# Performance work log

Hardware: AMD Instinct MI355X
Metric: run time of the kernel (lower is better)

## Reference

```python
import jax, jax.numpy as jnp
import numpy as np

B, S, D, H = 2, 4096, 1024, 16
HD = D // H
KCONV = 4


def _rmsnorm(x, scale, eps=1e-6):
    return x * jax.lax.rsqrt(jnp.mean(x * x, axis=-1, keepdims=True) + eps) * scale


def _l2norm(x, eps=1e-6):
    return x * jax.lax.rsqrt(jnp.sum(x * x, axis=-1, keepdims=True) + eps)


def _causal_dwconv_silu(x, w):
    # x: [B,S,D], w: [D,K] depthwise taps (tap K-1 multiplies x[t])
    k = w.shape[1]
    s = x.shape[1]
    xp = jnp.pad(x, ((0, 0), (k - 1, 0), (0, 0)))
    out = sum(xp[:, i:i + s, :] * w[:, i] for i in range(k))
    return jax.nn.silu(out)


def _p20_scan(x, decay_log, theta):
    # BLOCK_DIAGONAL_2 rotary-state linear recurrence: channels paired into
    # complex state, s_t = a * s_{t-1} + u_t with a = exp(-exp(decay_log) + i*theta).
    b, s, d = x.shape
    xc = x.reshape(b, s, d // 2, 2)
    u = jax.lax.complex(xc[..., 0], xc[..., 1])  # [B,S,D/2]
    a = jnp.exp(-jnp.exp(decay_log)) * jnp.exp(1j * theta)  # [D/2] complex, |a|<1

    def step(carry, u_t):
        st = carry * a + u_t
        return st, st

    _, ys = jax.lax.scan(step, jnp.zeros((b, d // 2), u.dtype), jnp.swapaxes(u, 0, 1))
    ys = jnp.swapaxes(ys, 0, 1)  # [B,S,D/2]
    return jnp.stack([ys.real, ys.imag], axis=-1).reshape(b, s, d)


def _gated_delta_rule(q, k, v, g, beta):
    # q,k,v: [B,S,H,Dh]; g,beta: [B,S,H]. State S: [B,H,K,V].
    scale = q.shape[-1] ** -0.5
    q = _l2norm(q)
    k = _l2norm(k)
    qt, kt, vt = (jnp.moveaxis(t, 1, 0) for t in (q, k, v))
    gt, bt = (jnp.moveaxis(t, 1, 0) for t in (g, beta))
    s0 = jnp.zeros((q.shape[0], q.shape[2], q.shape[3], v.shape[3]), v.dtype)

    def step(state, inp):
        q_t, k_t, v_t, g_t, b_t = inp
        state = state * jnp.exp(g_t)[..., None, None]
        v_err = (v_t - jnp.einsum('bhkv,bhk->bhv', state, k_t)) * b_t[..., None]
        state = state + jnp.einsum('bhk,bhv->bhkv', k_t, v_err)
        o_t = jnp.einsum('bhkv,bhk->bhv', state, q_t) * scale
        return state, o_t

    _, o = jax.lax.scan(step, s0, (qt, kt, vt, gt, bt))
    return jnp.moveaxis(o, 0, 1)  # [B,S,H,V]


def setup_inputs() -> dict:
    key = jax.random.key(0)
    ks = jax.random.split(key, 16)
    w = lambda k, shp, s=0.02: (jax.random.normal(k, shp, jnp.float32) * s)
    ctrl_out = 3 * D + 2 * H + D  # q,k,v,decay,beta,output_gate
    ctrl_b = jnp.concatenate([
        jnp.zeros((3 * D,), jnp.float32),
        jnp.full((H,), 1.5, jnp.float32),       # decay bias
        jnp.full((H,), -2.0, jnp.float32),      # beta bias
        jnp.full((D,), -1.5, jnp.float32),      # output gate bias
    ])
    # depthwise conv init: delta at last tap + small noise
    def conv_w(k):
        base = jnp.zeros((D, KCONV), jnp.float32).at[:, -1].set(1.0)
        return base + w(k, (D, KCONV), 0.02)
    return {
        'hidden': jax.random.normal(ks[0], (B, S, D), jnp.float32),
        'p20_decay_log': w(ks[1], (D // 2,), 1.0),
        'p20_theta': jax.random.uniform(ks[2], (D // 2,), jnp.float32, 0.0, 2.0 * np.pi),
        'ctrl_W': w(ks[3], (D, ctrl_out)),
        'ctrl_b': ctrl_b,
        'p20c_W': w(ks[4], (D, 3 * D), 0.001),  # 0.05-scaled init
        'qconv_w': conv_w(ks[5]),
        'kconv_w': conv_w(ks[6]),
        'vconv_w': conv_w(ks[7]),
        'mnorm_scale': jnp.ones((HD,), jnp.float32),
        'vnorm_scale': jnp.ones((D,), jnp.float32),
        'ramp_logit': jnp.full((D,), -4.595, jnp.float32),  # logit(0.01)
        'out_W': w(ks[8], (2 * D, D), 0.02),
        'out_b': jnp.zeros((D,), jnp.float32),
    }


def reference(hidden, p20_decay_log, p20_theta, ctrl_W, ctrl_b, p20c_W,
              qconv_w, kconv_w, vconv_w, mnorm_scale, vnorm_scale,
              ramp_logit, out_W, out_b):
    b, s, d = hidden.shape
    # P20 vector-state side channel
    p20_read = _p20_scan(hidden, p20_decay_log, p20_theta)
    normed_p20 = _rmsnorm(p20_read, vnorm_scale)
    p20_q, p20_k, p20_v = jnp.split(normed_p20 @ p20c_W, 3, axis=-1)
    ramp = jax.nn.sigmoid(ramp_logit)  # [D]
    # packed control projection
    ctrl = hidden @ ctrl_W + ctrl_b
    q_in, k_in, v_in, dec_in, beta_in, gate_in = jnp.split(
        ctrl, np.cumsum([d, d, d, H, H]).tolist(), axis=-1)
    # causal depthwise conv + SiLU
    q_in = _causal_dwconv_silu(q_in, qconv_w)
    k_in = _causal_dwconv_silu(k_in, kconv_w)
    v_in = _causal_dwconv_silu(v_in, vconv_w)
    # P20-conditioned heads
    queries = (q_in + ramp * p20_q).reshape(b, s, H, HD)
    keys = (k_in + ramp * p20_k).reshape(b, s, H, HD)
    values = (v_in + ramp * p20_v).reshape(b, s, H, HD)
    g = jax.nn.log_sigmoid(dec_in.astype(jnp.float32)).astype(hidden.dtype)  # [B,S,H]
    beta = jax.nn.sigmoid(beta_in)
    reads = _gated_delta_rule(queries, keys, values, g, beta)
    normed_reads = _rmsnorm(reads, mnorm_scale).reshape(b, s, d)
    fused = jnp.concatenate([normed_reads, normed_p20], axis=-1)
    projected = fused @ out_W + out_b
    return jax.nn.sigmoid(gate_in) * projected
```

## Files before the change

kernel.cpp:

```cpp
#include <hip/hip_runtime.h>
#include <hip/hip_bf16.h>
#include <stdint.h>

#define SEQ  4096
#define NH   16
#define HD   64

typedef __attribute__((ext_vector_type(8))) short bf16x8;
typedef __attribute__((ext_vector_type(4))) float f32x4;

__device__ __forceinline__ float bf2f(unsigned short u){
  union{unsigned u;float f;} v; v.u = ((unsigned)u)<<16; return v.f;
}
__device__ __forceinline__ unsigned short f2bf(float f){
  union{float f;unsigned u;} v; v.f=f;
  return (unsigned short)((v.u + 0x7fffu + ((v.u>>16)&1u))>>16);
}
__device__ __forceinline__ float sigm(float x){ return 1.f/(1.f+__expf(-x)); }
__device__ __forceinline__ f32x4 mfma16(bf16x8 a, bf16x8 b, f32x4 c){
  return __builtin_amdgcn_mfma_f32_16x16x32_bf16(a,b,c,0,0,0);
}
__device__ __forceinline__ void gll16(const void* g, void* l){
  __builtin_amdgcn_global_load_lds((const __attribute__((address_space(1))) void*)g,
                                   (__attribute__((address_space(3))) void*)l, 16, 0, 0);
}

__global__ void k_fill(float* __restrict__ p, float v, long n){
  long i = (long)blockIdx.x*blockDim.x + threadIdx.x;
  long stride = (long)gridDim.x*blockDim.x;
  for (; i<n; i+=stride) p[i] = v;
}

__global__ void k_cvt_bf16(const float* __restrict__ in, unsigned short* __restrict__ out){
  long i = ((long)blockIdx.x*256 + threadIdx.x)*4;
  float4 v = *(const float4*)(in+i);
  ushort4 o; o.x=f2bf(v.x); o.y=f2bf(v.y); o.z=f2bf(v.z); o.w=f2bf(v.w);
  *(ushort4*)(out+i) = o;
}

__global__ void k_transpose(const float* __restrict__ in, unsigned short* __restrict__ out,
                            int R, int Cin, int Cpad){
  __shared__ float t[32][33];
  int cb = blockIdx.x*32, rb = blockIdx.y*32;
  int tx = threadIdx.x & 31, ty = threadIdx.x >> 5;
  for (int k=0;k<32;k+=8){
    int r = rb+ty+k, c = cb+tx;
    t[ty+k][tx] = (c<Cin) ? in[(long)r*Cin + c] : 0.f;
  }
  __syncthreads();
  for (int k=0;k<32;k+=8){
    int c = cb+ty+k, r = rb+tx;
    if (c<Cpad) out[(long)c*R + r] = f2bf(t[tx][ty+k]);
  }
}

#define FOR16(F) F(0,0) F(0,1) F(0,2) F(0,3) F(1,0) F(1,1) F(1,2) F(1,3) \
                 F(2,0) F(2,1) F(2,2) F(2,3) F(3,0) F(3,1) F(3,2) F(3,3)
#define FOR4(F) F(0) F(1) F(2) F(3)
#define ACC(i,j) Ac##i##j

#define GEMM_CORE(A_,lda_,Bt_,ldb_,K_)                                         \
  __shared__ unsigned short Ab[3][4096];                                       \
  __shared__ unsigned short Bb[3][4096];                                       \
  const int tid=threadIdx.x, wid=tid>>6, l=tid&63;                             \
  const long m0=(long)blockIdx.y*128, n0=(long)blockIdx.x*128;                 \
  const int nk=(K_)>>5;                                                        \
  const int wm=(wid>>1)*64, wn=(wid&1)*64;                                     \
  const int srow0 = tid>>2;                                                    \
  const int schunk = (((tid&3) ^ ((tid>>2)&3))<<3);              \
  const unsigned short* gA0 = (A_) + (m0+srow0)*(lda_) + schunk;               \
  const unsigned short* gA1 = (A_) + (m0+64+srow0)*(lda_) + schunk;            \
  const unsigned short* gB0 = (Bt_) + (n0+srow0)*(ldb_) + schunk;              \
  const unsigned short* gB1 = (Bt_) + (n0+64+srow0)*(ldb_) + schunk;           \
  const int ldst0 = tid*16, ldst1 = 4096 + tid*16;    \
  f32x4 Ac00={0.f,0.f,0.f,0.f};                                                \
  f32x4 Ac01=Ac00,Ac02=Ac00,Ac03=Ac00,Ac10=Ac00,Ac11=Ac00,Ac12=Ac00,           \
        Ac13=Ac00,Ac20=Ac00,Ac21=Ac00,Ac22=Ac00,Ac23=Ac00,Ac30=Ac00,           \
        Ac31=Ac00,Ac32=Ac00,Ac33=Ac00;                                         \
                                            \
  gll16(gA0, (char*)&Ab[0][0]+ldst0); gll16(gA1, (char*)&Ab[0][0]+ldst1);      \
  gll16(gB0, (char*)&Bb[0][0]+ldst0); gll16(gB1, (char*)&Bb[0][0]+ldst1);      \
  gA0+=32; gA1+=32; gB0+=32; gB1+=32;                                          \
  gll16(gA0, (char*)&Ab[1][0]+ldst0); gll16(gA1, (char*)&Ab[1][0]+ldst1);      \
  gll16(gB0, (char*)&Bb[1][0]+ldst0); gll16(gB1, (char*)&Bb[1][0]+ldst1);      \
  gA0+=32; gA1+=32; gB0+=32; gB1+=32;                                          \
  int rb=0, sb=2;                                                              \
  const int sxor = (l&3)<<4;                                                   \
  const int rao0 = (wm+(l&15))*64 + (((l>>4)<<4) ^ sxor);                      \
  const int rbo0 = (wn+(l&15))*64 + (((l>>4)<<4) ^ sxor);                      \
  for (int kt=0; kt<nk; ++kt){                                                 \
    if (kt+1<nk) { asm volatile("s_waitcnt vmcnt(4)" ::: "memory"); }          \
    else         { asm volatile("s_waitcnt vmcnt(0)" ::: "memory"); }          \
    __builtin_amdgcn_sched_barrier(0);                                         \
    __builtin_amdgcn_s_barrier();                                              \
    __builtin_amdgcn_sched_barrier(0);                                         \
    if (kt+2<nk){                                                              \
      gll16(gA0, (char*)&Ab[sb][0]+ldst0); gll16(gA1, (char*)&Ab[sb][0]+ldst1);\
      gll16(gB0, (char*)&Bb[sb][0]+ldst0); gll16(gB1, (char*)&Bb[sb][0]+ldst1);\
      gA0+=32; gA1+=32; gB0+=32; gB1+=32;                                      \
    }                                                                          \
    const char* Apt=(const char*)&Ab[rb][0];                                   \
    const char* Bpt=(const char*)&Bb[rb][0];                                   \
    bf16x8 af0=*(const bf16x8*)(Apt+rao0);      bf16x8 bf0=*(const bf16x8*)(Bpt+rbo0);      \
    bf16x8 af1=*(const bf16x8*)(Apt+rao0+1024); bf16x8 bf1=*(const bf16x8*)(Bpt+rbo0+1024); \
    bf16x8 af2=*(const bf16x8*)(Apt+rao0+2048); bf16x8 bf2=*(const bf16x8*)(Bpt+rbo0+2048); \
    bf16x8 af3=*(const bf16x8*)(Apt+rao0+3072); bf16x8 bf3=*(const bf16x8*)(Bpt+rbo0+3072); \
    __builtin_amdgcn_s_setprio(1);                                             \
    Ac00=mfma16(af0,bf0,Ac00); Ac01=mfma16(af0,bf1,Ac01);                      \
    Ac02=mfma16(af0,bf2,Ac02); Ac03=mfma16(af0,bf3,Ac03);                      \
    Ac10=mfma16(af1,bf0,Ac10); Ac11=mfma16(af1,bf1,Ac11);                      \
    Ac12=mfma16(af1,bf2,Ac12); Ac13=mfma16(af1,bf3,Ac13);                      \
    Ac20=mfma16(af2,bf0,Ac20); Ac21=mfma16(af2,bf1,Ac21);                      \
    Ac22=mfma16(af2,bf2,Ac22); Ac23=mfma16(af2,bf3,Ac23);                      \
    Ac30=mfma16(af3,bf0,Ac30); Ac31=mfma16(af3,bf1,Ac31);                      \
    Ac32=mfma16(af3,bf2,Ac32); Ac33=mfma16(af3,bf3,Ac33);                      \
    __builtin_amdgcn_s_setprio(0);                                             \
    rb = (rb==2)?0:rb+1; sb = (sb==2)?0:sb+1;                                  \
  }

__global__ __launch_bounds__(256,2) void k_gemm(
  const unsigned short* __restrict__ A, int lda,
  const unsigned short* __restrict__ Bt, int ldb,
  unsigned short* Cb, float* Cf, int ldc,
  int K, int Nvalid,
  const float* __restrict__ bias,
  const unsigned short* __restrict__ gate, int gld)
{
  GEMM_CORE(A, lda, Bt, ldb, K)
#define EPI_GEN(mi,ni) {                                                       \
  const int gn=(int)n0+wn+ni*16+(l&15);                                        \
  if (gn<Nvalid){                                                              \
    _Pragma("unroll") for(int r=0;r<4;r++){                                    \
      const long gm=m0+wm+mi*16+((l>>4)<<2)+r;                                 \
      float v=ACC(mi,ni)[r];                                                   \
      if(bias) v+=bias[gn];                                                    \
      if(gate) v*=bf2f(gate[gm*gld+gn]);                                       \
      if(Cb) Cb[gm*ldc+gn]=f2bf(v); else Cf[gm*ldc+gn]=v; } } }
  FOR16(EPI_GEN)
#undef EPI_GEN
}

__global__ __launch_bounds__(256,2) void k_gemm_ctrl(
  const unsigned short* __restrict__ A, int lda,
  const unsigned short* __restrict__ Bt, int ldb,
  unsigned short* __restrict__ ctrl,
  float* __restrict__ gbuf, float* __restrict__ bbuf,
  unsigned short* __restrict__ gateb,
  const float* __restrict__ bias)
{
  GEMM_CORE(A, lda, Bt, ldb, 1024)
#define EPI_CTRL(mi,ni) {                                                      \
  const int gn=(int)n0+wn+ni*16+(l&15);                                        \
  if (gn<4128){                                                                \
    const float bs=bias[gn];                                                   \
    _Pragma("unroll") for(int r=0;r<4;r++){                                    \
      const long gm=m0+wm+mi*16+((l>>4)<<2)+r;                                 \
      float v=ACC(mi,ni)[r]+bs;                                                \
      if (gn<3072)      ctrl[gm*3072+gn]=f2bf(v);                              \
      else if (gn<3088) gbuf[gm*16+(gn-3072)]=                                 \
                          (v>=0.f)?-log1pf(__expf(-v)):(v-log1pf(__expf(v)));  \
      else if (gn<3104) bbuf[gm*16+(gn-3088)]=sigm(v);                         \
      else              gateb[gm*1024+(gn-3104)]=f2bf(sigm(v)); } } }
  FOR16(EPI_CTRL)
#undef EPI_CTRL
}

__global__ __launch_bounds__(256,2) void k_gemm_qkv(
  const unsigned short* __restrict__ A, int lda,
  const unsigned short* __restrict__ Bt, int ldb,
  const float* __restrict__ ramp,
  unsigned short* __restrict__ Qb, unsigned short* __restrict__ Kb,
  unsigned short* __restrict__ Vb)
{
  GEMM_CORE(A, lda, Bt, ldb, 1024)
  const int seg = (int)((n0 + wn) >> 10);
  unsigned short* Ob = (seg==0)?Qb:((seg==1)?Kb:Vb);
  const int dc0=((int)n0+wn+0*16+(l&15))&1023; const float sr0=sigm(ramp[dc0]);
  const int dc1=((int)n0+wn+1*16+(l&15))&1023; const float sr1=sigm(ramp[dc1]);
  const int dc2=((int)n0+wn+2*16+(l&15))&1023; const float sr2=sigm(ramp[dc2]);
  const int dc3=((int)n0+wn+3*16+(l&15))&1023; const float sr3=sigm(ramp[dc3]);
#define EPI_QKV(mi) {                                                          \
  _Pragma("unroll") for(int r=0;r<4;r++){                                      \
    const long gm=m0+wm+mi*16+((l>>4)<<2)+r;                                   \
    float v0=bf2f(Ob[gm*1024+dc0])+sr0*ACC(mi,0)[r];                           \
    float v1=bf2f(Ob[gm*1024+dc1])+sr1*ACC(mi,1)[r];                           \
    float v2=bf2f(Ob[gm*1024+dc2])+sr2*ACC(mi,2)[r];                           \
    float v3=bf2f(Ob[gm*1024+dc3])+sr3*ACC(mi,3)[r];                           \
    if (seg<2){                                                                \
      float ss=v0*v0+v1*v1+v2*v2+v3*v3;                                        \
      ss+=__shfl_xor(ss,1); ss+=__shfl_xor(ss,2);                              \
      ss+=__shfl_xor(ss,4); ss+=__shfl_xor(ss,8);                              \
      float rs=rsqrtf(ss+1e-6f); v0*=rs; v1*=rs; v2*=rs; v3*=rs; }             \
    Ob[gm*1024+dc0]=f2bf(v0); Ob[gm*1024+dc1]=f2bf(v1);                        \
    Ob[gm*1024+dc2]=f2bf(v2); Ob[gm*1024+dc3]=f2bf(v3); } }
  FOR4(EPI_QKV)
#undef EPI_QKV
}

__global__ void k_scan1(const float* __restrict__ hidden, const float* __restrict__ dlog,
                        const float* __restrict__ theta, float2* __restrict__ finals){
  int idx = blockIdx.x*256 + threadIdx.x;
  int ch = idx & 511; int chunk = (idx>>9) & 63; int b = idx>>15;
  float e = __expf(dlog[ch]); float r = __expf(-e);
  float th = theta[ch]; float ar = r*__cosf(th), ai = r*__sinf(th);
  const float2* src = (const float2*)hidden + ((long)b*SEQ + chunk*64)*512 + ch;
  float sr=0.f, si=0.f;
  for (int j=0;j<64;j++){
    float2 u = src[(long)j*512];
    float nr = sr*ar - si*ai + u.x;
    si = sr*ai + si*ar + u.y; sr = nr;
  }
  finals[idx] = make_float2(sr,si);
}
__global__ void k_scan2(const float* __restrict__ dlog, const float* __restrict__ theta,
                        const float2* __restrict__ finals, float2* __restrict__ carry, int nb){
  int idx = blockIdx.x*256+threadIdx.x; if (idx>=nb*512) return;
  int ch = idx & 511, b = idx>>9;
  float e = __expf(dlog[ch]); float r64 = __expf(-64.f*e);
  float ang = fmodf(64.f*theta[ch], 6.2831853071795864f);
  float cr = r64*__cosf(ang), ci = r64*__sinf(ang);
  float pr=0.f, pi=0.f;
  for (int c=0;c<64;c++){
    long o = ((long)b*64 + c)*512 + ch;
    carry[o] = make_float2(pr,pi);
    float2 f = finals[o];
    float nr = pr*cr - pi*ci + f.x;
    pi = pr*ci + pi*cr + f.y; pr = nr;
  }
}
__global__ void k_scan3(const float* __restrict__ hidden, const float* __restrict__ dlog,
                        const float* __restrict__ theta, const float2* __restrict__ carry,
                        unsigned short* __restrict__ p20){
  int idx = blockIdx.x*256 + threadIdx.x;
  int ch = idx & 511; int chunk = (idx>>9) & 63; int b = idx>>15;
  float e = __expf(dlog[ch]); float r = __expf(-e);
  float th = theta[ch]; float ar = r*__cosf(th), ai = r*__sinf(th);
  long toff = (long)b*SEQ + chunk*64;
  const float2* src = (const float2*)hidden + toff*512 + ch;
  unsigned short* dst = p20 + toff*1024 + 2*ch;
  float2 c0 = carry[idx];
  float sr=c0.x, si=c0.y;
  for (int j=0;j<64;j++){
    float2 u = src[(long)j*512];
    float nr = sr*ar - si*ai + u.x;
    si = sr*ai + si*ar + u.y; sr = nr;
    ushort2 o; o.x=f2bf(sr); o.y=f2bf(si);
    *(ushort2*)(dst + (long)j*1024) = o;
  }
}

__global__ __launch_bounds__(256) void k_rms_p20(const unsigned short* __restrict__ p20,
                        const float* __restrict__ vns, unsigned short* __restrict__ fused){
  long t = blockIdx.x;
  int d = threadIdx.x*4;
  ushort4 xu = *(const ushort4*)(p20 + t*1024 + d);
  float x0=bf2f(xu.x), x1=bf2f(xu.y), x2=bf2f(xu.z), x3=bf2f(xu.w);
  float ss = x0*x0 + x1*x1 + x2*x2 + x3*x3;
  for (int o=1;o<64;o<<=1) ss += __shfl_xor(ss, o);
  __shared__ float red[4];
  if ((threadIdx.x&63)==0) red[threadIdx.x>>6] = ss;
  __syncthreads();
  ss = red[0]+red[1]+red[2]+red[3];
  float rs = rsqrtf(ss*(1.f/1024.f) + 1e-6f);
  float4 s4 = *(const float4*)(vns + d);
  ushort4 o4;
  o4.x = f2bf(x0*rs*s4.x); o4.y = f2bf(x1*rs*s4.y);
  o4.z = f2bf(x2*rs*s4.z); o4.w = f2bf(x3*rs*s4.w);
  *(ushort4*)(fused + t*2048 + 1024 + d) = o4;
}

__global__ __launch_bounds__(256) void k_conv(const unsigned short* __restrict__ ctrl,
   const float* __restrict__ qw, const float* __restrict__ kw, const float* __restrict__ vw,
   unsigned short* __restrict__ Q, unsigned short* __restrict__ Kb, unsigned short* __restrict__ Vb){
  __shared__ unsigned short pan[19][256];
  int panel = blockIdx.x;
  int tb = blockIdx.y;
  int b = tb >> 8; int s0 = (tb & 255) * 16;
  int seg = panel >> 2; int d = (panel & 3)*256 + threadIdx.x;
  int c0 = panel*256;
  long base = (long)b*SEQ*3072;
  for (int rr=0; rr<19; rr++){
    int s = s0 - 3 + rr;
    pan[rr][threadIdx.x] = (s>=0) ? ctrl[base + (long)s*3072 + c0 + threadIdx.x] : (unsigned short)0;
  }
  __syncthreads();
  const float* cw = (seg==0)?qw:((seg==1)?kw:vw);
  float w0=cw[d*4], w1=cw[d*4+1], w2=cw[d*4+2], w3=cw[d*4+3];
  unsigned short* Ob = (seg==0)?Q:((seg==1)?Kb:Vb);
  for (int tk=0; tk<16; tk++){
    long t = (long)b*SEQ + s0 + tk;
    float x = bf2f(pan[tk][threadIdx.x])*w0 + bf2f(pan[tk+1][threadIdx.x])*w1
            + bf2f(pan[tk+2][threadIdx.x])*w2 + bf2f(pan[tk+3][threadIdx.x])*w3;
    x = x * sigm(x);
    Ob[t*1024 + d] = f2bf(x);
  }
}

__global__ __launch_bounds__(64,2) void k_phase1(
    const unsigned short* __restrict__ Kg, const unsigned short* __restrict__ Vg,
    const float* __restrict__ g, const float* __restrict__ beta,
    unsigned short* __restrict__ uvT, unsigned short* __restrict__ Wrm,
    unsigned short* __restrict__ Mc, unsigned short* __restrict__ BcT){
  __shared__ unsigned short Kc[64*64];
  __shared__ unsigned short Vc[64*64];
  __shared__ float Af[64*64];
  __shared__ float uTf[64*69];
  __shared__ float wTf[64*69];
  __shared__ float Gs[64], betl[64], bgam[64], decC[64];

  int bid = blockIdx.x; int bh = bid>>6, c = bid&63;
  int blocal = bh>>4, h = bh&15;
  long t0 = (long)blocal*SEQ + c*64;
  int l = threadIdx.x;
  long cbase = (long)bid*4096;

  float G = g[(t0+l)*16 + h];
  for (int o=1;o<64;o<<=1){ float n = __shfl_up(G,o); if (l>=o) G += n; }
  float bl = beta[(t0+l)*16+h];
  Gs[l]=G; betl[l]=bl; bgam[l]=bl*__expf(G);
  float G63 = __shfl(G,63);
  decC[l] = __expf(G63 - G);
  float GamC = __expf(G63);

  for (int it=0; it<8; it++){
    int bo = it*1024 + l*16;
    int row = bo>>7, bib = bo&127;
    int sb = bib ^ ((row&7)<<4);
    gll16(Kg + (t0+row)*1024 + h*64 + (sb>>1),  (char*)Kc + bo);
    gll16(Vg + (t0+row)*1024 + h*64 + (bib>>1), (char*)Vc + bo);
  }
  __syncthreads();

  bf16x8 kf[2][4];
  {
    int rr = l&15;
    #pragma unroll
    for (int t=0;t<4;t++)
      #pragma unroll
      for (int h2=0;h2<2;h2++){
        int row = t*16 + rr;
        int byt = row*128 + ((h2*64 + (l>>4)*16) ^ ((row&7)<<4));
        kf[h2][t] = *(const bf16x8*)((const char*)Kc + byt);
      }
  }
  #pragma unroll
  for (int ti=0;ti<4;ti++){
    #pragma unroll
    for (int tj=0;tj<4;tj++){
      f32x4 a = {0.f,0.f,0.f,0.f};
      a = mfma16(kf[0][ti], kf[0][tj], a);
      a = mfma16(kf[1][ti], kf[1][tj], a);
      int j = tj*16 + (l&15);
      float Gj = Gs[j];
      #pragma unroll
      for (int r=0;r<4;r++){
        int i = ti*16 + ((l>>4)<<2) + r;
        Af[i*64+j] = (j<i) ? betl[i]*a[r]*__expf(Gs[i]-Gj) : 0.f;
      }
    }
  }
  __syncthreads();

  {
    float uu[64], ww[64];
    #pragma unroll
    for (int i=0;i<64;i++){
      float ua = betl[i]*bf2f(Vc[i*64 + l]);
      float wa = bgam[i]*bf2f(*(const unsigned short*)((const char*)Kc + i*128 + ((2*l) ^ ((i&7)<<4))));
      #pragma unroll
      for (int j=0;j<i;j++){
        float av = Af[i*64+j];
        ua -= av*uu[j];
        wa -= av*ww[j];
      }
      uu[i] = ua; ww[i] = wa;
    }
    #pragma unroll
    for (int i=0;i<64;i++){
      uTf[l*69+i] = uu[i];
      wTf[l*69+i] = ww[i];
    }
  }
  __syncthreads();

  unsigned short* KTp = (unsigned short*)Af;
  for (int j=0;j<64;j++){
    float kv = bf2f(*(const unsigned short*)((const char*)Kc + j*128 + ((2*l) ^ ((j&7)<<4))));
    *(unsigned short*)((char*)KTp + l*128 + ((2*j) ^ ((l&7)<<4))) = f2bf(decC[j]*kv);
  }
  __syncthreads();

  auto ldfragKT = [&](int t, int h2)->bf16x8{
    int row = t*16 + (l&15);
    int byt = row*128 + ((h2*64 + (l>>4)*16) ^ ((row&7)<<4));
    return *(const bf16x8*)((const char*)KTp + byt);
  };
  auto ldfrag69 = [&](const float* base, int nrow, int h2)->bf16x8{
    const float* p = base + nrow*69 + h2*32 + ((l>>4)<<3);
    bf16x8 f;
    #pragma unroll
    for (int q=0;q<8;q++) f[q] = (short)f2bf(p[q]);
    return f;
  };

  #pragma unroll
  for (int to=0; to<4; to++){
    bf16x8 a0 = ldfragKT(to,0), a1 = ldfragKT(to,1);
    #pragma unroll
    for (int tn=0; tn<4; tn++){
      f32x4 accv = {0.f,0.f,0.f,0.f};
      accv = mfma16(a0, ldfrag69(wTf, tn*16+(l&15), 0), accv);
      accv = mfma16(a1, ldfrag69(wTf, tn*16+(l&15), 1), accv);
      int col = tn*16 + (l&15);
      #pragma unroll
      for (int r=0;r<4;r++){
        int row = to*16 + ((l>>4)<<2) + r;
        Mc[cbase + row*64 + col] = f2bf(((row==col)? GamC : 0.f) - accv[r]);
      }
    }
    #pragma unroll
    for (int tv=0; tv<4; tv++){
      f32x4 accv = {0.f,0.f,0.f,0.f};
      accv = mfma16(a0, ldfrag69(uTf, tv*16+(l&15), 0), accv);
      accv = mfma16(a1, ldfrag69(uTf, tv*16+(l&15), 1), accv);
      int v = tv*16 + (l&15);
      int k0 = to*16 + ((l>>4)<<2);
      short4 p;
      p.x=(short)f2bf(accv[0]); p.y=(short)f2bf(accv[1]);
      p.z=(short)f2bf(accv[2]); p.w=(short)f2bf(accv[3]);
      *(short4*)&BcT[cbase + v*64 + k0] = p;
    }
  }

  for (int rr=0; rr<64; rr++){
    uvT[cbase + rr*64 + l] = f2bf(uTf[rr*69 + l]);
    Wrm[cbase + rr*64 + l] = f2bf(wTf[l*69 + rr]);
  }
}

__global__ __launch_bounds__(64,2) void k_phase2(
    const unsigned short* __restrict__ Mc, const unsigned short* __restrict__ BcT,
    unsigned short* __restrict__ Sst){
  __shared__ unsigned short ST[64*64];
  int bh = blockIdx.x; int l = threadIdx.x;
  f32x4 acc[4][4];
  { f32x4 z = {0.f,0.f,0.f,0.f};
    #pragma unroll
    for (int i=0;i<4;i++)
      #pragma unroll
      for (int j=0;j<4;j++) acc[i][j]=z; }

  for (int c=0;c<64;c++){
    long cbase = ((long)bh*64 + c)*4096;
    #pragma unroll
    for (int ti=0;ti<4;ti++){
      #pragma unroll
      for (int tj=0;tj<4;tj++){
        int v = tj*16 + (l&15);
        int kd0 = ti*16 + ((l>>4)<<2);
        short4 p;
        p.x=(short)f2bf(acc[ti][tj][0]); p.y=(short)f2bf(acc[ti][tj][1]);
        p.z=(short)f2bf(acc[ti][tj][2]); p.w=(short)f2bf(acc[ti][tj][3]);
        *(short4*)&Sst[cbase + v*64 + kd0] = p;
        *(short4*)((char*)ST + v*128 + ((2*kd0) ^ ((v&7)<<4))) = p;
      }
    }
    __syncthreads();
    bf16x8 mf[2][4];
    #pragma unroll
    for (int ti=0;ti<4;ti++){
      int row = ti*16 + (l&15);
      mf[0][ti] = *(const bf16x8*)(Mc + cbase + row*64 + (l>>4)*8);
      mf[1][ti] = *(const bf16x8*)(Mc + cbase + row*64 + 32 + (l>>4)*8);
    }
    #pragma unroll
    for (int ti=0;ti<4;ti++)
      #pragma unroll
      for (int tj=0;tj<4;tj++){
        short4 bv = *(const short4*)&BcT[cbase + (long)(tj*16+(l&15))*64 + ti*16 + ((l>>4)<<2)];
        acc[ti][tj][0]=bf2f((unsigned short)bv.x); acc[ti][tj][1]=bf2f((unsigned short)bv.y);
        acc[ti][tj][2]=bf2f((unsigned short)bv.z); acc[ti][tj][3]=bf2f((unsigned short)bv.w);
      }
    bf16x8 sf[2][4];
    #pragma unroll
    for (int tj=0;tj<4;tj++){
      int v = tj*16 + (l&15);
      sf[0][tj] = *(const bf16x8*)((const char*)ST + v*128 + (((l>>4)*16) ^ ((v&7)<<4)));
      sf[1][tj] = *(const bf16x8*)((const char*)ST + v*128 + ((64+(l>>4)*16) ^ ((v&7)<<4)));
    }
    #pragma unroll
    for (int ti=0;ti<4;ti++)
      #pragma unroll
      for (int tj=0;tj<4;tj++){
        acc[ti][tj] = mfma16(mf[0][ti], sf[0][tj], acc[ti][tj]);
        acc[ti][tj] = mfma16(mf[1][ti], sf[1][tj], acc[ti][tj]);
      }
    __syncthreads();
  }
}

__global__ __launch_bounds__(64,2) void k_phase3(
  const unsigned short* __restrict__ Qg, const unsigned short* __restrict__ Kg,
  const float* __restrict__ g,
  const unsigned short* __restrict__ uvT, const unsigned short* __restrict__ Wrm,
  const unsigned short* __restrict__ Sst, const float* __restrict__ mns,
  unsigned short* __restrict__ fused){
  __shared__ unsigned short ST[64*64];
  __shared__ unsigned short QKl[64*64];
  __shared__ unsigned short uT[64*64];
  __shared__ float Gs[64];
  int bid = blockIdx.x; int bh = bid>>6, c = bid&63;
  int blocal = bh>>4, h = bh&15; long t0 = (long)blocal*SEQ + c*64;
  long cbase = (long)bid*4096;
  int l = threadIdx.x;

  float G = g[(t0+l)*16+h];
  for (int o=1;o<64;o<<=1){ float n=__shfl_up(G,o); if(l>=o) G+=n; }
  Gs[l]=G;

  #pragma unroll
  for (int it=0; it<16; it++){
    int flat = it*256 + l*4;
    int v = flat>>6, kd0 = flat&63;
    short4 s4 = *(const short4*)&Sst[cbase + flat];
    *(short4*)((char*)ST + v*128 + ((2*kd0) ^ ((v&7)<<4))) = s4;
  }
  __syncthreads();

  bf16x8 qf[2][4], kfr[2][4], sf[2][4];
  #pragma unroll
  for (int t=0;t<4;t++){
    long tr = t0 + t*16 + (l&15);
    qf[0][t]  = *(const bf16x8*)(Qg + tr*1024 + h*64 + (l>>4)*8);
    qf[1][t]  = *(const bf16x8*)(Qg + tr*1024 + h*64 + 32 + (l>>4)*8);
    kfr[0][t] = *(const bf16x8*)(Kg + tr*1024 + h*64 + (l>>4)*8);
    kfr[1][t] = *(const bf16x8*)(Kg + tr*1024 + h*64 + 32 + (l>>4)*8);
    int v = t*16 + (l&15);
    sf[0][t] = *(const bf16x8*)((const char*)ST + v*128 + (((l>>4)*16) ^ ((v&7)<<4)));
    sf[1][t] = *(const bf16x8*)((const char*)ST + v*128 + ((64+(l>>4)*16) ^ ((v&7)<<4)));
  }

  f32x4 qs[4][4];
  #pragma unroll
  for (int ti=0;ti<4;ti++)
    #pragma unroll
    for (int tj=0;tj<4;tj++){
      f32x4 a = {0.f,0.f,0.f,0.f};
      a = mfma16(qf[0][ti], sf[0][tj], a);
      a = mfma16(qf[1][ti], sf[1][tj], a);
      qs[ti][tj] = a;
    }

  #pragma unroll
  for (int ti=0;ti<4;ti++)
    #pragma unroll
    for (int tj=0;tj<4;tj++){
      f32x4 a = {0.f,0.f,0.f,0.f};
      a = mfma16(qf[0][ti], kfr[0][tj], a);
      a = mfma16(qf[1][ti], kfr[1][tj], a);
      int j = tj*16 + (l&15);
      float Gj = Gs[j];
      #pragma unroll
      for (int r=0;r<4;r++){
        int i = ti*16 + ((l>>4)<<2) + r;
        float v = (j<=i)? a[r]*__expf(Gs[i]-Gj) : 0.f;
        *(unsigned short*)((char*)QKl + i*128 + ((2*j) ^ ((i&7)<<4))) = f2bf(v);
      }
    }

  #pragma unroll
  for (int ti=0; ti<4; ti++){
    int irow = ti*16 + (l&15);
    bf16x8 w0 = *(const bf16x8*)(Wrm + cbase + irow*64 + (l>>4)*8);
    bf16x8 w1 = *(const bf16x8*)(Wrm + cbase + irow*64 + 32 + (l>>4)*8);
    #pragma unroll
    for (int tj=0; tj<4; tj++){
      f32x4 a = {0.f,0.f,0.f,0.f};
      a = mfma16(w0, sf[0][tj], a);
      a = mfma16(w1, sf[1][tj], a);
      int v = tj*16 + (l&15);
      int i0 = ti*16 + ((l>>4)<<2);
      short4 uv4 = *(const short4*)(uvT + cbase + (long)v*64 + i0);
      short4 p;
      p.x=(short)f2bf(bf2f((unsigned short)uv4.x) - a[0]);
      p.y=(short)f2bf(bf2f((unsigned short)uv4.y) - a[1]);
      p.z=(short)f2bf(bf2f((unsigned short)uv4.z) - a[2]);
      p.w=(short)f2bf(bf2f((unsigned short)uv4.w) - a[3]);
      *(short4*)((char*)uT + v*128 + ((2*i0) ^ ((v&7)<<4))) = p;
    }
  }
  __syncthreads();

  float mscale[4];
  #pragma unroll
  for (int tj=0;tj<4;tj++) mscale[tj] = mns[tj*16 + (l&15)];
  #pragma unroll
  for (int ti=0; ti<4; ti++){
    int row = ti*16 + (l&15);
    bf16x8 qk0 = *(const bf16x8*)((const char*)QKl + row*128 + (((l>>4)*16) ^ ((row&7)<<4)));
    bf16x8 qk1 = *(const bf16x8*)((const char*)QKl + row*128 + ((64+(l>>4)*16) ^ ((row&7)<<4)));
    #pragma unroll
    for (int tj=0; tj<4; tj++){
      int v = tj*16 + (l&15);
      bf16x8 u0 = *(const bf16x8*)((const char*)uT + v*128 + (((l>>4)*16) ^ ((v&7)<<4)));
      bf16x8 u1 = *(const bf16x8*)((const char*)uT + v*128 + ((64+(l>>4)*16) ^ ((v&7)<<4)));
      f32x4 a;
      #pragma unroll
      for (int r=0;r<4;r++){
        float gam = __expf(Gs[ti*16 + ((l>>4)<<2) + r]);
        a[r] = qs[ti][tj][r]*gam;
      }
      a = mfma16(qk0,u0,a);
      a = mfma16(qk1,u1,a);
      qs[ti][tj] = a;
    }
  }
  #pragma unroll
  for (int ti=0; ti<4; ti++){
    #pragma unroll
    for (int r=0; r<4; r++){
      float ss = 0.f;
      #pragma unroll
      for (int tj=0;tj<4;tj++){ float v = qs[ti][tj][r]*0.125f; ss += v*v; }
      ss += __shfl_xor(ss,1); ss += __shfl_xor(ss,2); ss += __shfl_xor(ss,4); ss += __shfl_xor(ss,8);
      float rs = rsqrtf(ss*(1.f/64.f) + 1e-6f);
      long t = t0 + ti*16 + ((l>>4)<<2) + r;
      #pragma unroll
      for (int tj=0;tj<4;tj++){
        float on = qs[ti][tj][r]*0.125f*rs*mscale[tj];
        fused[t*2048 + h*64 + tj*16 + (l&15)] = f2bf(on);
      }
    }
  }
}

extern "C" void kernel_launch(void* const* d_in, const int* in_sizes, int n_in,
                              void* d_out, int out_size, void* d_ws, size_t ws_size,
                              hipStream_t stream){
  (void)in_sizes; (void)n_in;
  const float* hidden = (const float*)d_in[0];
  const float* dlog   = (const float*)d_in[1];
  const float* theta  = (const float*)d_in[2];
  const float* ctrlW  = (const float*)d_in[3];
  const float* ctrlb  = (const float*)d_in[4];
  const float* p20cW  = (const float*)d_in[5];
  const float* qw     = (const float*)d_in[6];
  const float* kw     = (const float*)d_in[7];
  const float* vw     = (const float*)d_in[8];
  const float* mns    = (const float*)d_in[9];
  const float* vns    = (const float*)d_in[10];
  const float* ramp   = (const float*)d_in[11];
  const float* outW   = (const float*)d_in[12];
  const float* outb   = (const float*)d_in[13];
  float* out = (float*)d_out;

  struct Bufs {
    unsigned short *ctrl, *uvT, *Wrm, *Mc;
    unsigned short *Qb, *Kb, *Vb, *fused;
    unsigned short *E_hid, *E_p20, *BcT;
    unsigned short *Sst, *gateb, *ctrlWT, *p20WT, *outWT;
    float2 *finals, *carry; float *gbuf, *bbuf;
    size_t need;
  };
  auto mk = [&](size_t NT)->Bufs{
    Bufs B; size_t off=0;
    auto tk=[&](size_t n)->char*{ char* p=(char*)d_ws+off; off += (n+255)&~(size_t)255; return p; };
    char* Rctrl = tk(NT*3072*2);
    B.ctrl=(unsigned short*)Rctrl;
    B.uvT=(unsigned short*)Rctrl; B.Wrm=B.uvT + NT*1024; B.Mc=B.Wrm + NT*1024;
    char* Rqkv = tk(NT*1024*2*3);
    B.Qb=(unsigned short*)Rqkv; B.Kb=B.Qb+NT*1024; B.Vb=B.Kb+NT*1024;
    B.fused=(unsigned short*)tk(NT*2048*2);
    char* RE = tk(NT*1024*2);
    B.E_hid=(unsigned short*)RE; B.E_p20=(unsigned short*)RE; B.BcT=(unsigned short*)RE;
    B.Sst=(unsigned short*)tk(NT*1024*2);
    B.gateb=(unsigned short*)tk(NT*1024*2);
    B.ctrlWT=(unsigned short*)tk((size_t)4224*1024*2);
    B.p20WT=(unsigned short*)tk((size_t)3072*1024*2);
    B.outWT=(unsigned short*)tk((size_t)1024*2048*2);
    B.finals=(float2*)tk(NT*64);
    B.carry=(float2*)tk(NT*64);
    B.gbuf=(float*)tk(NT*16*4);
    B.bbuf=(float*)tk(NT*16*4);
    B.need=off;
    return B;
  };

  Bufs Bf = mk(8192);
  Bufs Bh = mk(4096);
  Bufs B; size_t NT; int nb;
  if      (Bf.need <= ws_size){ B=Bf; NT=8192; nb=2; }
  else if (Bh.need <= ws_size){ B=Bh; NT=4096; nb=1; }
  else {
    k_fill<<<2048,256,0,stream>>>(out, (float)((double)ws_size), (long)out_size);
    return;
  }

  k_transpose<<<dim3(132,32),256,0,stream>>>(ctrlW, B.ctrlWT, 1024, 4128, 4224);
  k_transpose<<<dim3(96,32), 256,0,stream>>>(p20cW, B.p20WT, 1024, 3072, 3072);
  k_transpose<<<dim3(32,64), 256,0,stream>>>(outW,  B.outWT, 2048, 1024, 1024);

  for (int b0=0; b0<2; b0+=nb){
    const float* hidb = hidden + (size_t)b0*SEQ*1024;
    float* outp = out + (size_t)b0*SEQ*1024;
    k_cvt_bf16<<<(int)NT,256,0,stream>>>(hidb, B.E_hid);
    k_gemm_ctrl<<<dim3(33,NT/128),256,0,stream>>>(B.E_hid,1024, B.ctrlWT,1024,
                                                  B.ctrl, B.gbuf, B.bbuf, B.gateb, ctrlb);
    k_scan1<<<nb*128,256,0,stream>>>(hidb,dlog,theta,B.finals);
    k_scan2<<<nb*2, 256,0,stream>>>(dlog,theta,B.finals,B.carry,nb);
    k_scan3<<<nb*128,256,0,stream>>>(hidb,dlog,theta,B.carry,B.E_p20);
    k_rms_p20<<<(int)NT,256,0,stream>>>(B.E_p20,vns,B.fused);
    k_conv<<<dim3(12,NT/16),256,0,stream>>>(B.ctrl,qw,kw,vw,B.Qb,B.Kb,B.Vb);
    k_gemm_qkv<<<dim3(24,NT/128),256,0,stream>>>(B.fused+1024,2048, B.p20WT,1024,
                                                 ramp, B.Qb,B.Kb,B.Vb);
    k_phase1<<<(int)(NT/4),64,0,stream>>>(B.Kb,B.Vb,B.gbuf,B.bbuf,B.uvT,B.Wrm,B.Mc,B.BcT);
    k_phase2<<<nb*16,64,0,stream>>>(B.Mc,B.BcT,B.Sst);
    k_phase3<<<(int)(NT/4),64,0,stream>>>(B.Qb,B.Kb,B.gbuf,B.uvT,B.Wrm,B.Sst,mns,B.fused);
    k_gemm<<<dim3(8,NT/128),256,0,stream>>>(B.fused,2048, B.outWT,2048,
                                            nullptr,outp,1024, 2048,1024, outb, B.gateb,1024);
  }
}
```

Before: 623.8 us.

## Use 256x256 eight-wave GEMM tiles for ctrl and qkv projections

Adds a new GEMM core with 256x256 output tiles, 512 threads (8 waves each holding a 128x64 subtile), BK=64 double-buffered direct-to-LDS loads, staged loads interleaved with MFMA phases and s_setprio. It is used for the ctrl and p20-qkv projections, replacing the 128x128 triple-buffered core, to raise arithmetic intensity and cut global/LDS traffic per FLOP. The cost is more LDS (128KB) and registers, fewer blocks (17x32 and 12x32), and the ctrl weight must be padded to 4352 columns, which wastes some work in the last column tile.

```diff
diff --git a/kernel.cpp b/kernel.cpp
--- a/kernel.cpp
+++ b/kernel.cpp
@@ -54,10 +54,187 @@
   }
 }
 
+#define FOR84(F) \
+ F(0,0) F(0,1) F(0,2) F(0,3) F(1,0) F(1,1) F(1,2) F(1,3) \
+ F(2,0) F(2,1) F(2,2) F(2,3) F(3,0) F(3,1) F(3,2) F(3,3) \
+ F(4,0) F(4,1) F(4,2) F(4,3) F(5,0) F(5,1) F(5,2) F(5,3) \
+ F(6,0) F(6,1) F(6,2) F(6,3) F(7,0) F(7,1) F(7,2) F(7,3)
+#define FOR8(F) F(0) F(1) F(2) F(3) F(4) F(5) F(6) F(7)
 #define FOR16(F) F(0,0) F(0,1) F(0,2) F(0,3) F(1,0) F(1,1) F(1,2) F(1,3) \
                  F(2,0) F(2,1) F(2,2) F(2,3) F(3,0) F(3,1) F(3,2) F(3,3)
 #define FOR4(F) F(0) F(1) F(2) F(3)
 #define ACC(i,j) Ac##i##j
+
+#define MROW(Ak0,Ak1,CA,CB,B0k0,B0k1,B1k0,B1k1) \
+  CA = mfma16(Ak0,B0k0,CA); CA = mfma16(Ak1,B0k1,CA); \
+  CB = mfma16(Ak0,B1k0,CB); CB = mfma16(Ak1,B1k1,CB);
+
+#define SBAR0 __builtin_amdgcn_sched_barrier(0)
+
+#define GEMM256_CORE(A_,lda_,Bt_,ldb_,K_)                                      \
+  __shared__ unsigned short Ab[2][16384];                                      \
+  __shared__ unsigned short Bb[2][16384];                                      \
+  const int tid=threadIdx.x, wid=tid>>6, l=tid&63;                             \
+  const long m0=(long)blockIdx.y*256, n0=(long)blockIdx.x*256;                 \
+  const int nt=(K_)>>6;                                                        \
+  const int wr=wid>>2, wc=wid&3;                                               \
+  const int srow=(tid>>3), sch=((tid&7)^((tid>>3)&7))*8;                       \
+  const unsigned short* pA0=(A_)+(m0+srow)*(lda_)+sch;                         \
+  const unsigned short* pA1=(A_)+(m0+64+srow)*(lda_)+sch;                      \
+  const unsigned short* pA2=(A_)+(m0+128+srow)*(lda_)+sch;                     \
+  const unsigned short* pA3=(A_)+(m0+192+srow)*(lda_)+sch;                     \
+  const unsigned short* pB0=(Bt_)+(n0+srow)*(ldb_)+sch;                        \
+  const unsigned short* pB1=(Bt_)+(n0+64+srow)*(ldb_)+sch;                     \
+  const unsigned short* pB2=(Bt_)+(n0+128+srow)*(ldb_)+sch;                    \
+  const unsigned short* pB3=(Bt_)+(n0+192+srow)*(ldb_)+sch;                    \
+  char* LA=(char*)&Ab[0][0]; char* LB=(char*)&Bb[0][0];                        \
+  const int dst=tid*16;                                                        \
+  f32x4 Ac00={0.f,0.f,0.f,0.f};                                                \
+  f32x4 Ac01=Ac00,Ac02=Ac00,Ac03=Ac00,Ac10=Ac00,Ac11=Ac00,Ac12=Ac00,Ac13=Ac00, \
+        Ac20=Ac00,Ac21=Ac00,Ac22=Ac00,Ac23=Ac00,Ac30=Ac00,Ac31=Ac00,Ac32=Ac00, \
+        Ac33=Ac00,Ac40=Ac00,Ac41=Ac00,Ac42=Ac00,Ac43=Ac00,Ac50=Ac00,Ac51=Ac00, \
+        Ac52=Ac00,Ac53=Ac00,Ac60=Ac00,Ac61=Ac00,Ac62=Ac00,Ac63=Ac00,Ac70=Ac00, \
+        Ac71=Ac00,Ac72=Ac00,Ac73=Ac00;                                         \
+                                   \
+  gll16(pA0,LA+dst); gll16(pA1,LA+8192+dst);                                   \
+  gll16(pA2,LA+16384+dst); gll16(pA3,LA+24576+dst);                            \
+  gll16(pB0,LB+dst); gll16(pB1,LB+8192+dst);                                   \
+  gll16(pB2,LB+16384+dst); gll16(pB3,LB+24576+dst);                            \
+  pA0+=64; pA1+=64; pA2+=64; pA3+=64; pB0+=64; pB1+=64; pB2+=64; pB3+=64;      \
+  gll16(pA0,LA+32768+dst); gll16(pA1,LA+40960+dst);                            \
+  gll16(pA2,LA+49152+dst); gll16(pA3,LA+57344+dst);                            \
+  gll16(pB0,LB+32768+dst); gll16(pB1,LB+40960+dst);                            \
+  gll16(pB2,LB+49152+dst); gll16(pB3,LB+57344+dst);                            \
+  pA0+=64; pA1+=64; pA2+=64; pA3+=64; pB0+=64; pB1+=64; pB2+=64; pB3+=64;      \
+  const int rbA=(wr*128+(l&15))*128, rbB=(wc*64+(l&15))*128;                   \
+  const int cx0=(((l>>4)^(l&7))<<4), cx1=cx0^64;                               \
+  for (int t=0;t<nt;++t){                                                      \
+    if (t==0) { asm volatile("s_waitcnt vmcnt(8)":::"memory"); }               \
+    else      { asm volatile("s_waitcnt vmcnt(0)":::"memory"); }               \
+    SBAR0; __builtin_amdgcn_s_barrier(); SBAR0;                                \
+    const char* Apt=(const char*)&Ab[0][0]+(t&1)*32768;                        \
+    const char* Bpt=(const char*)&Bb[0][0]+(t&1)*32768;                        \
+    const int ob=(1-(t&1))*32768;                                              \
+    const bool iss=(t>=1)&&(t+1<nt);                                           \
+       \
+    bf16x8 Af0k0=*(const bf16x8*)(Apt+rbA+cx0);                                \
+    bf16x8 Af0k1=*(const bf16x8*)(Apt+rbA+cx1);                                \
+    bf16x8 Af1k0=*(const bf16x8*)(Apt+rbA+2048+cx0);                           \
+    bf16x8 Af1k1=*(const bf16x8*)(Apt+rbA+2048+cx1);                           \
+    bf16x8 Af2k0=*(const bf16x8*)(Apt+rbA+4096+cx0);                           \
+    bf16x8 Af2k1=*(const bf16x8*)(Apt+rbA+4096+cx1);                           \
+    bf16x8 Af3k0=*(const bf16x8*)(Apt+rbA+6144+cx0);                           \
+    bf16x8 Af3k1=*(const bf16x8*)(Apt+rbA+6144+cx1);                           \
+    bf16x8 Bx0k0=*(const bf16x8*)(Bpt+rbB+cx0);                                \
+    bf16x8 Bx0k1=*(const bf16x8*)(Bpt+rbB+cx1);                                \
+    bf16x8 Bx1k0=*(const bf16x8*)(Bpt+rbB+2048+cx0);                           \
+    bf16x8 Bx1k1=*(const bf16x8*)(Bpt+rbB+2048+cx1);                           \
+    if (iss){ gll16(pA0,LA+ob+dst); gll16(pA1,LA+ob+8192+dst);                 \
+              gll16(pA2,LA+ob+16384+dst); gll16(pA3,LA+ob+24576+dst); }        \
+    __builtin_amdgcn_s_setprio(1);                                             \
+    MROW(Af0k0,Af0k1, Ac00,Ac01, Bx0k0,Bx0k1,Bx1k0,Bx1k1)                      \
+    MROW(Af1k0,Af1k1, Ac10,Ac11, Bx0k0,Bx0k1,Bx1k0,Bx1k1)                      \
+    MROW(Af2k0,Af2k1, Ac20,Ac21, Bx0k0,Bx0k1,Bx1k0,Bx1k1)                      \
+    MROW(Af3k0,Af3k1, Ac30,Ac31, Bx0k0,Bx0k1,Bx1k0,Bx1k1)                      \
+    __builtin_amdgcn_s_setprio(0);                                             \
+    __builtin_amdgcn_s_barrier(); SBAR0;                                       \
+              \
+    bf16x8 By0k0=*(const bf16x8*)(Bpt+rbB+4096+cx0);                           \
+    bf16x8 By0k1=*(const bf16x8*)(Bpt+rbB+4096+cx1);                           \
+    bf16x8 By1k0=*(const bf16x8*)(Bpt+rbB+6144+cx0);                           \
+    bf16x8 By1k1=*(const bf16x8*)(Bpt+rbB+6144+cx1);                           \
+    if (iss){ gll16(pB0,LB+ob+dst); gll16(pB1,LB+ob+8192+dst);                 \
+              gll16(pB2,LB+ob+16384+dst); gll16(pB3,LB+ob+24576+dst);          \
+              pA0+=64; pA1+=64; pA2+=64; pA3+=64;                              \
+              pB0+=64; pB1+=64; pB2+=64; pB3+=64; }                            \
+    __builtin_amdgcn_s_setprio(1);                                             \
+    MROW(Af0k0,Af0k1, Ac02,Ac03, By0k0,By0k1,By1k0,By1k1)                      \
+    MROW(Af1k0,Af1k1, Ac12,Ac13, By0k0,By0k1,By1k0,By1k1)                      \
+    MROW(Af2k0,Af2k1, Ac22,Ac23, By0k0,By0k1,By1k0,By1k1)                      \
+    MROW(Af3k0,Af3k1, Ac32,Ac33, By0k0,By0k1,By1k0,By1k1)                      \
+    __builtin_amdgcn_s_setprio(0);                                             \
+    __builtin_amdgcn_s_barrier(); SBAR0;                                       \
+                      \
+    Af0k0=*(const bf16x8*)(Apt+rbA+8192+cx0);                                  \
+    Af0k1=*(const bf16x8*)(Apt+rbA+8192+cx1);                                  \
+    Af1k0=*(const bf16x8*)(Apt+rbA+10240+cx0);                                 \
+    Af1k1=*(const bf16x8*)(Apt+rbA+10240+cx1);                                 \
+    Af2k0=*(const bf16x8*)(Apt+rbA+12288+cx0);                                 \
+    Af2k1=*(const bf16x8*)(Apt+rbA+12288+cx1);                                 \
+    Af3k0=*(const bf16x8*)(Apt+rbA+14336+cx0);                                 \
+    Af3k1=*(const bf16x8*)(Apt+rbA+14336+cx1);                                 \
+    __builtin_amdgcn_s_setprio(1);                                             \
+    MROW(Af0k0,Af0k1, Ac42,Ac43, By0k0,By0k1,By1k0,By1k1)                      \
+    MROW(Af1k0,Af1k1, Ac52,Ac53, By0k0,By0k1,By1k0,By1k1)                      \
+    MROW(Af2k0,Af2k1, Ac62,Ac63, By0k0,By0k1,By1k0,By1k1)                      \
+    MROW(Af3k0,Af3k1, Ac72,Ac73, By0k0,By0k1,By1k0,By1k1)                      \
+    __builtin_amdgcn_s_setprio(0);                                             \
+    __builtin_amdgcn_s_barrier(); SBAR0;                                       \
+                                         \
+    __builtin_amdgcn_s_setprio(1);                                             \
+    MROW(Af0k0,Af0k1, Ac40,Ac41, Bx0k0,Bx0k1,Bx1k0,Bx1k1)                      \
+    MROW(Af1k0,Af1k1, Ac50,Ac51, Bx0k0,Bx0k1,Bx1k0,Bx1k1)                      \
+    MROW(Af2k0,Af2k1, Ac60,Ac61, Bx0k0,Bx0k1,Bx1k0,Bx1k1)                      \
+    MROW(Af3k0,Af3k1, Ac70,Ac71, Bx0k0,Bx0k1,Bx1k0,Bx1k1)                      \
+    __builtin_amdgcn_s_setprio(0);                                             \
+  }
+
+__global__ __launch_bounds__(512,2) void k_gemm_ctrl(
+  const unsigned short* __restrict__ A, int lda,
+  const unsigned short* __restrict__ Bt, int ldb,
+  unsigned short* __restrict__ ctrl,
+  float* __restrict__ gbuf, float* __restrict__ bbuf,
+  unsigned short* __restrict__ gateb,
+  const float* __restrict__ bias)
+{
+  GEMM256_CORE(A, lda, Bt, ldb, 1024)
+#define EPI_CTRL(fm,fn) {                                                      \
+  const int gn=(int)n0+wc*64+fn*16+(l&15);                                     \
+  if (gn<4128){                                                                \
+    const float bs=bias[gn];                                                   \
+    _Pragma("unroll") for(int r=0;r<4;r++){                                    \
+      const long gm=m0+wr*128+fm*16+((l>>4)<<2)+r;                             \
+      float v=ACC(fm,fn)[r]+bs;                                                \
+      if (gn<3072)      ctrl[gm*3072+gn]=f2bf(v);                              \
+      else if (gn<3088) gbuf[gm*16+(gn-3072)]=                                 \
+                          (v>=0.f)?-log1pf(__expf(-v)):(v-log1pf(__expf(v)));  \
+      else if (gn<3104) bbuf[gm*16+(gn-3088)]=sigm(v);                         \
+      else              gateb[gm*1024+(gn-3104)]=f2bf(sigm(v)); } } }
+  FOR84(EPI_CTRL)
+#undef EPI_CTRL
+}
+
+__global__ __launch_bounds__(512,2) void k_gemm_qkv(
+  const unsigned short* __restrict__ A, int lda,
+  const unsigned short* __restrict__ Bt, int ldb,
+  const float* __restrict__ ramp,
+  unsigned short* __restrict__ Qb, unsigned short* __restrict__ Kb,
+  unsigned short* __restrict__ Vb)
+{
+  GEMM256_CORE(A, lda, Bt, ldb, 1024)
+  const int seg = (int)((n0 + wc*64) >> 10);
+  unsigned short* Ob = (seg==0)?Qb:((seg==1)?Kb:Vb);
+  const int dc0=((int)n0+wc*64+ 0+(l&15))&1023; const float sr0=sigm(ramp[dc0]);
+  const int dc1=((int)n0+wc*64+16+(l&15))&1023; const float sr1=sigm(ramp[dc1]);
+  const int dc2=((int)n0+wc*64+32+(l&15))&1023; const float sr2=sigm(ramp[dc2]);
+  const int dc3=((int)n0+wc*64+48+(l&15))&1023; const float sr3=sigm(ramp[dc3]);
+#define EPI_QKV(fm) {                                                          \
+  _Pragma("unroll") for(int r=0;r<4;r++){                                      \
+    const long gm=m0+wr*128+fm*16+((l>>4)<<2)+r;                               \
+    float v0=bf2f(Ob[gm*1024+dc0])+sr0*ACC(fm,0)[r];                           \
+    float v1=bf2f(Ob[gm*1024+dc1])+sr1*ACC(fm,1)[r];                           \
+    float v2=bf2f(Ob[gm*1024+dc2])+sr2*ACC(fm,2)[r];                           \
+    float v3=bf2f(Ob[gm*1024+dc3])+sr3*ACC(fm,3)[r];                           \
+    if (seg<2){                                                                \
+      float ss=v0*v0+v1*v1+v2*v2+v3*v3;                                        \
+      ss+=__shfl_xor(ss,1); ss+=__shfl_xor(ss,2);                              \
+      ss+=__shfl_xor(ss,4); ss+=__shfl_xor(ss,8);                              \
+      float rs=rsqrtf(ss+1e-6f); v0*=rs; v1*=rs; v2*=rs; v3*=rs; }             \
+    Ob[gm*1024+dc0]=f2bf(v0); Ob[gm*1024+dc1]=f2bf(v1);                        \
+    Ob[gm*1024+dc2]=f2bf(v2); Ob[gm*1024+dc3]=f2bf(v3); } }
+  FOR8(EPI_QKV)
+#undef EPI_QKV
+}
 
 #define GEMM_CORE(A_,lda_,Bt_,ldb_,K_)                                         \
   __shared__ unsigned short Ab[3][4096];                                       \
@@ -67,17 +244,16 @@
   const int nk=(K_)>>5;                                                        \
   const int wm=(wid>>1)*64, wn=(wid&1)*64;                                     \
   const int srow0 = tid>>2;                                                    \
-  const int schunk = (((tid&3) ^ ((tid>>2)&3))<<3);              \
+  const int schunk = (((tid&3) ^ ((tid>>2)&3))<<3);                            \
   const unsigned short* gA0 = (A_) + (m0+srow0)*(lda_) + schunk;               \
   const unsigned short* gA1 = (A_) + (m0+64+srow0)*(lda_) + schunk;            \
   const unsigned short* gB0 = (Bt_) + (n0+srow0)*(ldb_) + schunk;              \
   const unsigned short* gB1 = (Bt_) + (n0+64+srow0)*(ldb_) + schunk;           \
-  const int ldst0 = tid*16, ldst1 = 4096 + tid*16;    \
+  const int ldst0 = tid*16, ldst1 = 4096 + tid*16;                             \
   f32x4 Ac00={0.f,0.f,0.f,0.f};                                                \
   f32x4 Ac01=Ac00,Ac02=Ac00,Ac03=Ac00,Ac10=Ac00,Ac11=Ac00,Ac12=Ac00,           \
         Ac13=Ac00,Ac20=Ac00,Ac21=Ac00,Ac22=Ac00,Ac23=Ac00,Ac30=Ac00,           \
         Ac31=Ac00,Ac32=Ac00,Ac33=Ac00;                                         \
-                                            \
   gll16(gA0, (char*)&Ab[0][0]+ldst0); gll16(gA1, (char*)&Ab[0][0]+ldst1);      \
   gll16(gB0, (char*)&Bb[0][0]+ldst0); gll16(gB1, (char*)&Bb[0][0]+ldst1);      \
   gA0+=32; gA1+=32; gB0+=32; gB1+=32;                                          \
@@ -140,63 +316,6 @@
 #undef EPI_GEN
 }
 
-__global__ __launch_bounds__(256,2) void k_gemm_ctrl(
-  const unsigned short* __restrict__ A, int lda,
-  const unsigned short* __restrict__ Bt, int ldb,
-  unsigned short* __restrict__ ctrl,
-  float* __restrict__ gbuf, float* __restrict__ bbuf,
-  unsigned short* __restrict__ gateb,
-  const float* __restrict__ bias)
-{
-  GEMM_CORE(A, lda, Bt, ldb, 1024)
-#define EPI_CTRL(mi,ni) {                                                      \
-  const int gn=(int)n0+wn+ni*16+(l&15);                                        \
-  if (gn<4128){                                                                \
-    const float bs=bias[gn];                                                   \
-    _Pragma("unroll") for(int r=0;r<4;r++){                                    \
-      const long gm=m0+wm+mi*16+((l>>4)<<2)+r;                                 \
-      float v=ACC(mi,ni)[r]+bs;                                                \
-      if (gn<3072)      ctrl[gm*3072+gn]=f2bf(v);                              \
-      else if (gn<3088) gbuf[gm*16+(gn-3072)]=                                 \
-                          (v>=0.f)?-log1pf(__expf(-v)):(v-log1pf(__expf(v)));  \
-      else if (gn<3104) bbuf[gm*16+(gn-3088)]=sigm(v);                         \
-      else              gateb[gm*1024+(gn-3104)]=f2bf(sigm(v)); } } }
-  FOR16(EPI_CTRL)
-#undef EPI_CTRL
-}
-
-__global__ __launch_bounds__(256,2) void k_gemm_qkv(
-  const unsigned short* __restrict__ A, int lda,
-  const unsigned short* __restrict__ Bt, int ldb,
-  const float* __restrict__ ramp,
-  unsigned short* __restrict__ Qb, unsigned short* __restrict__ Kb,
-  unsigned short* __restrict__ Vb)
-{
-  GEMM_CORE(A, lda, Bt, ldb, 1024)
-  const int seg = (int)((n0 + wn) >> 10);
-  unsigned short* Ob = (seg==0)?Qb:((seg==1)?Kb:Vb);
-  const int dc0=((int)n0+wn+0*16+(l&15))&1023; const float sr0=sigm(ramp[dc0]);
-  const int dc1=((int)n0+wn+1*16+(l&15))&1023; const float sr1=sigm(ramp[dc1]);
-  const int dc2=((int)n0+wn+2*16+(l&15))&1023; const float sr2=sigm(ramp[dc2]);
-  const int dc3=((int)n0+wn+3*16+(l&15))&1023; const float sr3=sigm(ramp[dc3]);
-#define EPI_QKV(mi) {                                                          \
-  _Pragma("unroll") for(int r=0;r<4;r++){                                      \
-    const long gm=m0+wm+mi*16+((l>>4)<<2)+r;                                   \
-    float v0=bf2f(Ob[gm*1024+dc0])+sr0*ACC(mi,0)[r];                           \
-    float v1=bf2f(Ob[gm*1024+dc1])+sr1*ACC(mi,1)[r];                           \
-    float v2=bf2f(Ob[gm*1024+dc2])+sr2*ACC(mi,2)[r];                           \
-    float v3=bf2f(Ob[gm*1024+dc3])+sr3*ACC(mi,3)[r];                           \
-    if (seg<2){                                                                \
-      float ss=v0*v0+v1*v1+v2*v2+v3*v3;                                        \
-      ss+=__shfl_xor(ss,1); ss+=__shfl_xor(ss,2);                              \
-      ss+=__shfl_xor(ss,4); ss+=__shfl_xor(ss,8);                              \
-      float rs=rsqrtf(ss+1e-6f); v0*=rs; v1*=rs; v2*=rs; v3*=rs; }             \
-    Ob[gm*1024+dc0]=f2bf(v0); Ob[gm*1024+dc1]=f2bf(v1);                        \
-    Ob[gm*1024+dc2]=f2bf(v2); Ob[gm*1024+dc3]=f2bf(v3); } }
-  FOR4(EPI_QKV)
-#undef EPI_QKV
-}
-
 __global__ void k_scan1(const float* __restrict__ hidden, const float* __restrict__ dlog,
                         const float* __restrict__ theta, float2* __restrict__ finals){
   int idx = blockIdx.x*256 + threadIdx.x;
@@ -325,8 +444,8 @@
   for (int it=0; it<8; it++){
     int bo = it*1024 + l*16;
     int row = bo>>7, bib = bo&127;
-    int sb = bib ^ ((row&7)<<4);
-    gll16(Kg + (t0+row)*1024 + h*64 + (sb>>1),  (char*)Kc + bo);
+    int sb2 = bib ^ ((row&7)<<4);
+    gll16(Kg + (t0+row)*1024 + h*64 + (sb2>>1),  (char*)Kc + bo);
     gll16(Vg + (t0+row)*1024 + h*64 + (bib>>1), (char*)Vc + bo);
   }
   __syncthreads();
@@ -675,7 +794,7 @@
     B.E_hid=(unsigned short*)RE; B.E_p20=(unsigned short*)RE; B.BcT=(unsigned short*)RE;
     B.Sst=(unsigned short*)tk(NT*1024*2);
     B.gateb=(unsigned short*)tk(NT*1024*2);
-    B.ctrlWT=(unsigned short*)tk((size_t)4224*1024*2);
+    B.ctrlWT=(unsigned short*)tk((size_t)4352*1024*2);
     B.p20WT=(unsigned short*)tk((size_t)3072*1024*2);
     B.outWT=(unsigned short*)tk((size_t)1024*2048*2);
     B.finals=(float2*)tk(NT*64);
@@ -696,7 +815,7 @@
     return;
   }
 
-  k_transpose<<<dim3(132,32),256,0,stream>>>(ctrlW, B.ctrlWT, 1024, 4128, 4224);
+  k_transpose<<<dim3(136,32),256,0,stream>>>(ctrlW, B.ctrlWT, 1024, 4128, 4352);
   k_transpose<<<dim3(96,32), 256,0,stream>>>(p20cW, B.p20WT, 1024, 3072, 3072);
   k_transpose<<<dim3(32,64), 256,0,stream>>>(outW,  B.outWT, 2048, 1024, 1024);
 
@@ -704,14 +823,14 @@
     const float* hidb = hidden + (size_t)b0*SEQ*1024;
     float* outp = out + (size_t)b0*SEQ*1024;
     k_cvt_bf16<<<(int)NT,256,0,stream>>>(hidb, B.E_hid);
-    k_gemm_ctrl<<<dim3(33,NT/128),256,0,stream>>>(B.E_hid,1024, B.ctrlWT,1024,
+    k_gemm_ctrl<<<dim3(17,NT/256),512,0,stream>>>(B.E_hid,1024, B.ctrlWT,1024,
                                                   B.ctrl, B.gbuf, B.bbuf, B.gateb, ctrlb);
     k_scan1<<<nb*128,256,0,stream>>>(hidb,dlog,theta,B.finals);
     k_scan2<<<nb*2, 256,0,stream>>>(dlog,theta,B.finals,B.carry,nb);
     k_scan3<<<nb*128,256,0,stream>>>(hidb,dlog,theta,B.carry,B.E_p20);
     k_rms_p20<<<(int)NT,256,0,stream>>>(B.E_p20,vns,B.fused);
     k_conv<<<dim3(12,NT/16),256,0,stream>>>(B.ctrl,qw,kw,vw,B.Qb,B.Kb,B.Vb);
-    k_gemm_qkv<<<dim3(24,NT/128),256,0,stream>>>(B.fused+1024,2048, B.p20WT,1024,
+    k_gemm_qkv<<<dim3(12,NT/256),512,0,stream>>>(B.fused+1024,2048, B.p20WT,1024,
                                                  ramp, B.Qb,B.Kb,B.Vb);
     k_phase1<<<(int)(NT/4),64,0,stream>>>(B.Kb,B.Vb,B.gbuf,B.bbuf,B.uvT,B.Wrm,B.Mc,B.BcT);
     k_phase2<<<nb*16,64,0,stream>>>(B.Mc,B.BcT,B.Sst);
```

Measured after the change: 676.9 us. 1.09x slower.
